# Kernel optimization log

Measured on AMD Instinct MI355X. Metric: run time of the kernel, lower is better.

The kernel has to match this reference:

```python
import jax, jax.numpy as jnp
import numpy as np

N, D, B = 50000, 256, 2048
SIGMA = 1.0
SIGMA2 = SIGMA * SIGMA  # module stores np.square(sigma)


def setup_inputs() -> dict:
    key = jax.random.key(0)
    k1, k2, k3, k4 = jax.random.split(key, 4)
    x = jax.random.normal(k1, (B, D), dtype=jnp.float32)
    data_set = jax.random.normal(k2, (N, D), dtype=jnp.float32)
    # labels are +/-1
    data_labels = jnp.where(jax.random.uniform(k3, (N,)) < 0.5, -1.0, 1.0).astype(jnp.float32)
    # lambdas initialized to ones in the module; use small positive noise around 1/n scale
    lambdas = jax.random.uniform(k4, (N,), dtype=jnp.float32) * (2.0 / N)
    b = jnp.ones((1,), dtype=jnp.float32)
    return {"x": x, "data_set": data_set, "data_labels": data_labels,
            "lambdas": lambdas, "b": b}


def reference(x, data_set, data_labels, lambdas, b):
    x2 = jnp.sum(x * x, axis=1, keepdims=True)            # [B,1]
    s2 = jnp.sum(data_set * data_set, axis=1)             # [N]
    cross = jnp.einsum('bd,nd->bn', x, data_set)          # [B,N]
    sqdist = x2 + s2[None, :] - 2.0 * cross               # [B,N]
    K = jnp.exp(-sqdist / (2.0 * SIGMA2))                 # rbf kernel [B,N]
    w = data_labels * jax.nn.relu(lambdas)                # [N]
    return jnp.tanh(K @ w + b)                            # [B]
```

## Files before the change

### kernel.cpp

```cpp
#include <hip/hip_runtime.h>
#include <hip/hip_bf16.h>
#include <hip/hip_fp8.h>
#include <math.h>

#define NPTS 50000
#define DIM  256
#define BQ   2048
#define NPAD 50048

#define CH   32
#define NCH32 1564
#define NG   64
#define LOG2E 1.4426950408889634f

#define WS_ACC 0
#define WS_X2  2048
#define WS_T   4096
#define WS_SGN 54144
#define WS_XB  104192
#define WS_SB  366336
#define WS_TOTAL_BYTES (6772480ull * 4ull)

#define V1_ACC 0
#define V1_X2  2048
#define V1_S2  4096
#define V1_W   54096

typedef __bf16 bf16x8 __attribute__((ext_vector_type(8)));
typedef __bf16 bf16x4 __attribute__((ext_vector_type(4)));
typedef float  f32x4  __attribute__((ext_vector_type(4)));
typedef float  f32x16 __attribute__((ext_vector_type(16)));
typedef int    i32x4  __attribute__((ext_vector_type(4)));
typedef int    i32x8  __attribute__((ext_vector_type(8)));
typedef unsigned int u32;
typedef unsigned char u8;

__device__ __forceinline__ float fast_exp2(float v) {
#if __has_builtin(__builtin_amdgcn_exp2f)
  return __builtin_amdgcn_exp2f(v);
#else
  return exp2f(v);
#endif
}

__device__ __forceinline__ void async_copy16(const void* g, void* l) {
  __builtin_amdgcn_global_load_lds(
      (const __attribute__((address_space(1))) u32*)g,
      (__attribute__((address_space(3))) u32*)l, 16, 0, 0);
}

__device__ __forceinline__ u32 pack_fp8x4(float4 v) {
#if __has_builtin(__builtin_amdgcn_cvt_pk_fp8_f32)
  int pk = __builtin_amdgcn_cvt_pk_fp8_f32(v.x, v.y, 0, false);
  pk = __builtin_amdgcn_cvt_pk_fp8_f32(v.z, v.w, pk, true);
  return (u32)pk;
#else
  __hip_fp8_e4m3 a(v.x), b(v.y), c(v.z), d(v.w);
  return (u32)a.__x | ((u32)b.__x << 8) | ((u32)c.__x << 16) | ((u32)d.__x << 24);
#endif
}


__global__ __launch_bounds__(256) void svm_precvt10(
    const float* __restrict__ x, const float* __restrict__ s,
    const float* __restrict__ labels, const float* __restrict__ lambdas,
    float* __restrict__ ws) {
  const int wid  = blockIdx.x * 4 + (threadIdx.x >> 6);
  const int lane = threadIdx.x & 63;
  u8* xb8 = (u8*)(ws + WS_XB);
  u8* sb8 = (u8*)(ws + WS_SB);

  if (blockIdx.x < 8) ws[WS_ACC + blockIdx.x * 256 + threadIdx.x] = 0.0f;

  if (wid < NPAD) {
    float4 v = make_float4(0.f, 0.f, 0.f, 0.f);
    if (wid < NPTS)
      v = reinterpret_cast<const float4*>(s + (size_t)wid * DIM)[lane];
    ((u32*)(sb8 + (size_t)wid * DIM))[lane] = pack_fp8x4(v);
    float ss = v.x * v.x + v.y * v.y + v.z * v.z + v.w * v.w;
    #pragma unroll
    for (int off = 32; off > 0; off >>= 1) ss += __shfl_xor(ss, off);
    if (lane == 0) {
      float s2h = 0.5f * LOG2E * ss;
      float lam = (wid < NPTS) ? lambdas[wid] : 0.0f;
      float lab = (wid < NPTS) ? labels[wid] : 1.0f;
      float mag = lam > 0.0f ? lam : 0.0f;
      ws[WS_T + wid]   = (mag > 0.0f) ? s2h - log2f(mag) : __builtin_inff();
      ws[WS_SGN + wid] = lab;
    }
  } else if (wid < NPAD + BQ) {
    int r = wid - NPAD;
    float4 v = reinterpret_cast<const float4*>(x + (size_t)r * DIM)[lane];
    ((u32*)(xb8 + (size_t)r * DIM))[lane] = pack_fp8x4(v);
    float ss = v.x * v.x + v.y * v.y + v.z * v.z + v.w * v.w;
    #pragma unroll
    for (int off = 32; off > 0; off >>= 1) ss += __shfl_xor(ss, off);
    if (lane == 0) ws[WS_X2 + r] = 0.5f * LOG2E * ss;
  }
}

__global__ __launch_bounds__(256, 2) void svm_main20(float* __restrict__ ws) {
  __shared__ u8 sB[3][8192];

  const u8* xb8 = (const u8*)(ws + WS_XB);
  const u8* sb8 = (const u8*)(ws + WS_SB);
  const float* x2g = ws + WS_X2;
  const float* tg  = ws + WS_T;
  const float* sgg = ws + WS_SGN;
  float* accOut    = ws + WS_ACC;

  const int t    = threadIdx.x;
  const int wave = t >> 6;
  const int lane = t & 63;
  const int l32  = lane & 31;
  const int hk   = lane >> 5;
  const int g    = blockIdx.x & (NG - 1);
  const int mt   = blockIdx.x >> 6;
  const int m0   = mt * 256;
  const int c0   = (NCH32 * g) / NG;
  const int c1   = (NCH32 * (g + 1)) / NG;

#define STAGE20(buf, cc)                                                      \
  do {                                                                        \
    _Pragma("unroll")                                                         \
    for (int i = 0; i < 2; ++i) {                                             \
      int p  = wave * 2 + i;                                        \
      int kt = p >> 1;                                              \
      int h  = p & 1;                                                         \
      int r  = h * 16 + (lane >> 2);                                          \
      int q  = (lane & 3) ^ ((r >> 1) & 3);                                   \
      const u8* src = sb8 + (size_t)((cc) * CH + r) * DIM + kt * 64 + q * 16; \
      async_copy16(src, &sB[(buf)][kt * 2048 + h * 1024 + lane * 16]);        \
    }                                                                         \
  } while (0)

  STAGE20(0, c0);
  STAGE20(1, c0 + 1);

  i32x8 afr[2][4];
  #pragma unroll
  for (int mi = 0; mi < 2; ++mi)
    #pragma unroll
    for (int kt = 0; kt < 4; ++kt) {
      const u8* ap = xb8 + (size_t)(m0 + wave * 64 + mi * 32 + l32) * DIM
                         + kt * 64 + hk * 32;
      i32x4 a0 = *reinterpret_cast<const i32x4*>(ap);
      i32x4 a1 = *reinterpret_cast<const i32x4*>(ap + 16);
      afr[mi][kt] = __builtin_shufflevector(a0, a1, 0, 1, 2, 3, 4, 5, 6, 7);
    }
  #pragma unroll
  for (int mi = 0; mi < 2; ++mi)
    #pragma unroll
    for (int kt = 0; kt < 4; ++kt)
      asm volatile("" : "+v"(afr[mi][kt]));

  float runAcc0[16], runAcc1[16];
  #pragma unroll
  for (int i = 0; i < 16; ++i) { runAcc0[i] = 0.0f; runAcc1[i] = 0.0f; }

  asm volatile("s_waitcnt vmcnt(2)" ::: "memory");
  __builtin_amdgcn_s_barrier();

  int cur = 0;
  for (int c = c0; c < c1; ++c) {
    float tt = tg[c * CH + l32];
    float sg = sgg[c * CH + l32];
    __builtin_amdgcn_sched_barrier(0);

    {
      int c2 = c + 2;
      if (c2 < c1) {
        int b2 = cur + 2; if (b2 >= 3) b2 -= 3;
        STAGE20(b2, c2);
      }
    }

    f32x16 acc0 = (f32x16)(0.0f), acc1 = (f32x16)(0.0f);
    const u8* bufB = &sB[cur][0];
    #pragma unroll
    for (int kt = 0; kt < 4; ++kt) {
      int s0 = ((l32 << 2) | (hk << 1)) ^ ((l32 >> 1) & 3);
      const u8* bp = bufB + kt * 2048;
      i32x4 lo = *reinterpret_cast<const i32x4*>(bp + s0 * 16);
      i32x4 hi = *reinterpret_cast<const i32x4*>(bp + (s0 ^ 1) * 16);
      i32x8 bfr = __builtin_shufflevector(lo, hi, 0, 1, 2, 3, 4, 5, 6, 7);
      acc0 = __builtin_amdgcn_mfma_scale_f32_32x32x64_f8f6f4(
          afr[0][kt], bfr, acc0, 0, 0, 0, 0x7F7F7F7F, 0, 0x7F7F7F7F);
      acc1 = __builtin_amdgcn_mfma_scale_f32_32x32x64_f8f6f4(
          afr[1][kt], bfr, acc1, 0, 0, 0, 0x7F7F7F7F, 0, 0x7F7F7F7F);
    }

    #pragma unroll
    for (int reg = 0; reg < 16; ++reg)
      runAcc0[reg] = __builtin_fmaf(
          sg, fast_exp2(__builtin_fmaf(acc0[reg], LOG2E, -tt)), runAcc0[reg]);
    #pragma unroll
    for (int reg = 0; reg < 16; ++reg)
      runAcc1[reg] = __builtin_fmaf(
          sg, fast_exp2(__builtin_fmaf(acc1[reg], LOG2E, -tt)), runAcc1[reg]);

    __builtin_amdgcn_s_barrier();
    asm volatile("" ::: "memory");
    cur = (cur + 1 < 3) ? cur + 1 : 0;
  }

  #pragma unroll
  for (int reg = 0; reg < 16; ++reg) {
    float v = runAcc0[reg];
    v += __shfl_xor(v, 1);
    v += __shfl_xor(v, 2);
    v += __shfl_xor(v, 4);
    v += __shfl_xor(v, 8);
    v += __shfl_xor(v, 16);
    if (l32 == 0) {
      int row = m0 + wave * 64 + (reg & 3) + 8 * (reg >> 2) + 4 * hk;
      atomicAdd(&accOut[row], fast_exp2(-x2g[row]) * v);
    }
  }
  #pragma unroll
  for (int reg = 0; reg < 16; ++reg) {
    float v = runAcc1[reg];
    v += __shfl_xor(v, 1);
    v += __shfl_xor(v, 2);
    v += __shfl_xor(v, 4);
    v += __shfl_xor(v, 8);
    v += __shfl_xor(v, 16);
    if (l32 == 0) {
      int row = m0 + wave * 64 + 32 + (reg & 3) + 8 * (reg >> 2) + 4 * hk;
      atomicAdd(&accOut[row], fast_exp2(-x2g[row]) * v);
    }
  }
#undef STAGE20
}


#define BK 32

__global__ __launch_bounds__(256) void svm_precompute(
    const float* __restrict__ x, const float* __restrict__ s,
    const float* __restrict__ labels, const float* __restrict__ lambdas,
    float* __restrict__ ws) {
  int wid  = blockIdx.x * 4 + (threadIdx.x >> 6);
  int lane = threadIdx.x & 63;
  const float* src;
  if (wid < NPTS)           src = s + (size_t)wid * DIM;
  else if (wid < NPTS + BQ) src = x + (size_t)(wid - NPTS) * DIM;
  else return;
  float4 v = reinterpret_cast<const float4*>(src)[lane];
  float ss = v.x * v.x + v.y * v.y + v.z * v.z + v.w * v.w;
  #pragma unroll
  for (int off = 32; off > 0; off >>= 1) ss += __shfl_xor(ss, off);
  if (lane == 0) {
    if (wid < NPTS) {
      ws[V1_S2 + wid] = ss;
      float lam = lambdas[wid];
      ws[V1_W + wid] = labels[wid] * (lam > 0.0f ? lam : 0.0f);
    } else {
      ws[V1_X2 + (wid - NPTS)] = ss;
    }
  }
}

__global__ __launch_bounds__(256) void svm_main(
    const float* __restrict__ x, const float* __restrict__ s,
    const float* __restrict__ ws) {
  __shared__ __bf16 sA[128 * BK];
  __shared__ __bf16 sB2[128 * BK];

  const int t    = threadIdx.x;
  const int wave = t >> 6;
  const int lane = t & 63;
  const int quad = lane >> 4;
  const int l16  = lane & 15;
  const int wm   = (wave & 1) * 64;
  const int wn   = (wave >> 1) * 64;
  const int bRow0 = blockIdx.y * 128;
  const int n0    = blockIdx.x * 128;

  f32x4 acc[4][4];
  #pragma unroll
  for (int i = 0; i < 4; ++i)
    #pragma unroll
    for (int j = 0; j < 4; ++j)
      acc[i][j] = (f32x4)(0.0f);

  for (int kt = 0; kt < DIM / BK; ++kt) {
    const int k0 = kt * BK;
    __syncthreads();
    #pragma unroll
    for (int i = 0; i < 4; ++i) {
      int slot = t + i * 256;
      int r  = slot >> 3;
      int c4 = slot & 7;
      float4 va = reinterpret_cast<const float4*>(
          x + (size_t)(bRow0 + r) * DIM + k0)[c4];
      bf16x4 ha = { (__bf16)va.x, (__bf16)va.y, (__bf16)va.z, (__bf16)va.w };
      *reinterpret_cast<bf16x4*>(&sA[r * BK + c4 * 4]) = ha;

      int nrow = n0 + r;
      float4 vb = make_float4(0.f, 0.f, 0.f, 0.f);
      if (nrow < NPTS)
        vb = reinterpret_cast<const float4*>(
            s + (size_t)nrow * DIM + k0)[c4];
      bf16x4 hb = { (__bf16)vb.x, (__bf16)vb.y, (__bf16)vb.z, (__bf16)vb.w };
      *reinterpret_cast<bf16x4*>(&sB2[r * BK + c4 * 4]) = hb;
    }
    __syncthreads();

    bf16x8 af[4], bfv[4];
    #pragma unroll
    for (int mi = 0; mi < 4; ++mi)
      af[mi] = *reinterpret_cast<const bf16x8*>(
          &sA[(wm + mi * 16 + l16) * BK + quad * 8]);
    #pragma unroll
    for (int ni = 0; ni < 4; ++ni)
      bfv[ni] = *reinterpret_cast<const bf16x8*>(
          &sB2[(wn + ni * 16 + l16) * BK + quad * 8]);
    #pragma unroll
    for (int mi = 0; mi < 4; ++mi)
      #pragma unroll
      for (int ni = 0; ni < 4; ++ni)
        acc[mi][ni] = __builtin_amdgcn_mfma_f32_16x16x32_bf16(
            af[mi], bfv[ni], acc[mi][ni], 0, 0, 0);
  }

  const float* x2g = ws + V1_X2;
  const float* s2g = ws + V1_S2;
  const float* wg  = ws + V1_W;
  float* accOut    = (float*)ws + V1_ACC;

  float s2v[4], wv[4];
  #pragma unroll
  for (int ni = 0; ni < 4; ++ni) {
    int n = n0 + wn + ni * 16 + l16;
    bool ok = n < NPTS;
    s2v[ni] = ok ? s2g[n] : 0.0f;
    wv[ni]  = ok ? wg[n]  : 0.0f;
  }
  #pragma unroll
  for (int mi = 0; mi < 4; ++mi) {
    const int mbase = wm + mi * 16 + quad * 4;
    #pragma unroll
    for (int reg = 0; reg < 4; ++reg) {
      float x2r = x2g[bRow0 + mbase + reg];
      float ps = 0.0f;
      #pragma unroll
      for (int ni = 0; ni < 4; ++ni) {
        float cc = acc[mi][ni][reg];
        ps += __expf(__builtin_fmaf(-0.5f, x2r + s2v[ni], cc)) * wv[ni];
      }
      ps += __shfl_xor(ps, 1);
      ps += __shfl_xor(ps, 2);
      ps += __shfl_xor(ps, 4);
      ps += __shfl_xor(ps, 8);
      if (l16 == 0) atomicAdd(&accOut[bRow0 + mbase + reg], ps);
    }
  }
}


__global__ __launch_bounds__(256) void svm_finalize(
    const float* __restrict__ ws, const float* __restrict__ bias,
    float* __restrict__ out) {
  int i = blockIdx.x * 256 + threadIdx.x;
  if (i < BQ) out[i] = tanhf(ws[i] + bias[0]);
}

extern "C" void kernel_launch(void* const* d_in, const int* in_sizes, int n_in,
                              void* d_out, int out_size, void* d_ws, size_t ws_size,
                              hipStream_t stream) {
  const float* x       = (const float*)d_in[0];
  const float* s       = (const float*)d_in[1];
  const float* labels  = (const float*)d_in[2];
  const float* lambdas = (const float*)d_in[3];
  const float* bias    = (const float*)d_in[4];
  float* out = (float*)d_out;
  float* ws  = (float*)d_ws;

  if (ws_size >= WS_TOTAL_BYTES) {
    svm_precvt10<<<(NPAD + BQ + 3) / 4, 256, 0, stream>>>(x, s, labels, lambdas, ws);
    svm_main20<<<8 * NG, 256, 0, stream>>>(ws);
  } else {
    hipMemsetAsync(ws, 0, BQ * sizeof(float), stream);
    svm_precompute<<<(NPTS + BQ + 3) / 4, 256, 0, stream>>>(x, s, labels, lambdas, ws);
    dim3 grid(391, BQ / 128);
    svm_main<<<grid, 256, 0, stream>>>(x, s, ws);
  }
  svm_finalize<<<BQ / 256, 256, 0, stream>>>(ws, bias, out);
}
```

Measured before the change: 144.9 us.

## Process two chunks per barrier with a four-buffer LDS ring

The main loop now handles two 32-point chunks per iteration and uses a 4-deep LDS ring instead of 3, so it needs half as many workgroup barriers and has more independent MFMA/exp work between syncs. A tail handles an odd chunk count. The precompute step also switches log2f to the hardware log intrinsic, which is slightly less accurate. LDS use per block grows from 24KB to 32KB, which may matter for occupancy at two blocks per CU.

```diff
diff --git a/kernel.cpp b/kernel.cpp
--- a/kernel.cpp
+++ b/kernel.cpp
@@ -40,6 +40,14 @@
   return __builtin_amdgcn_exp2f(v);
 #else
   return exp2f(v);
+#endif
+}
+
+__device__ __forceinline__ float fast_log2(float v) {
+#if __has_builtin(__builtin_amdgcn_logf)
+  return __builtin_amdgcn_logf(v);
+#else
+  return __log2f(v);
 #endif
 }
 
@@ -85,7 +93,7 @@
       float lam = (wid < NPTS) ? lambdas[wid] : 0.0f;
       float lab = (wid < NPTS) ? labels[wid] : 1.0f;
       float mag = lam > 0.0f ? lam : 0.0f;
-      ws[WS_T + wid]   = (mag > 0.0f) ? s2h - log2f(mag) : __builtin_inff();
+      ws[WS_T + wid]   = (mag > 0.0f) ? s2h - fast_log2(mag) : __builtin_inff();
       ws[WS_SGN + wid] = lab;
     }
   } else if (wid < NPAD + BQ) {
@@ -99,8 +107,8 @@
   }
 }
 
-__global__ __launch_bounds__(256, 2) void svm_main20(float* __restrict__ ws) {
-  __shared__ u8 sB[3][8192];
+__global__ __launch_bounds__(256, 2) void svm_main23(float* __restrict__ ws) {
+  __shared__ u8 sB[4][8192];
 
   const u8* xb8 = (const u8*)(ws + WS_XB);
   const u8* sb8 = (const u8*)(ws + WS_SB);
@@ -120,7 +128,7 @@
   const int c0   = (NCH32 * g) / NG;
   const int c1   = (NCH32 * (g + 1)) / NG;
 
-#define STAGE20(buf, cc)                                                      \
+#define STAGE23(buf, cc)                                                      \
   do {                                                                        \
     _Pragma("unroll")                                                         \
     for (int i = 0; i < 2; ++i) {                                             \
@@ -134,8 +142,36 @@
     }                                                                         \
   } while (0)
 
-  STAGE20(0, c0);
-  STAGE20(1, c0 + 1);
+#define CHUNK23(BUFIDX, CC)                                                   \
+  do {                                                                        \
+    f32x16 acc0 = (f32x16)(0.0f), acc1 = (f32x16)(0.0f);                      \
+    const u8* bufB = &sB[(BUFIDX)][0];                                        \
+    _Pragma("unroll")                                                         \
+    for (int kt = 0; kt < 4; ++kt) {                                          \
+      int s0 = ((l32 << 2) | (hk << 1)) ^ ((l32 >> 1) & 3);                   \
+      const u8* bp = bufB + kt * 2048;                                        \
+      i32x4 lo = *reinterpret_cast<const i32x4*>(bp + s0 * 16);               \
+      i32x4 hi = *reinterpret_cast<const i32x4*>(bp + (s0 ^ 1) * 16);         \
+      i32x8 bfr = __builtin_shufflevector(lo, hi, 0, 1, 2, 3, 4, 5, 6, 7);    \
+      acc0 = __builtin_amdgcn_mfma_scale_f32_32x32x64_f8f6f4(                 \
+          afr[0][kt], bfr, acc0, 0, 0, 0, 0x7F7F7F7F, 0, 0x7F7F7F7F);         \
+      acc1 = __builtin_amdgcn_mfma_scale_f32_32x32x64_f8f6f4(                 \
+          afr[1][kt], bfr, acc1, 0, 0, 0, 0x7F7F7F7F, 0, 0x7F7F7F7F);         \
+    }                                                                         \
+    _Pragma("unroll")                                                         \
+    for (int reg = 0; reg < 16; ++reg)                                        \
+      runAcc0[reg] = __builtin_fmaf(                                          \
+          sg_##CC, fast_exp2(__builtin_fmaf(acc0[reg], LOG2E, -tt_##CC)),     \
+          runAcc0[reg]);                                                      \
+    _Pragma("unroll")                                                         \
+    for (int reg = 0; reg < 16; ++reg)                                        \
+      runAcc1[reg] = __builtin_fmaf(                                          \
+          sg_##CC, fast_exp2(__builtin_fmaf(acc1[reg], LOG2E, -tt_##CC)),     \
+          runAcc1[reg]);                                                      \
+  } while (0)
+
+  STAGE23(0, c0);
+  STAGE23(1, c0 + 1);
 
   i32x8 afr[2][4];
   #pragma unroll
@@ -162,46 +198,29 @@
   __builtin_amdgcn_s_barrier();
 
   int cur = 0;
-  for (int c = c0; c < c1; ++c) {
-    float tt = tg[c * CH + l32];
-    float sg = sgg[c * CH + l32];
+  int c = c0;
+  for (; c + 1 < c1; c += 2) {
+    float tt_a = tg[c * CH + l32];
+    float sg_a = sgg[c * CH + l32];
     __builtin_amdgcn_sched_barrier(0);
-
-    {
-      int c2 = c + 2;
-      if (c2 < c1) {
-        int b2 = cur + 2; if (b2 >= 3) b2 -= 3;
-        STAGE20(b2, c2);
-      }
-    }
-
-    f32x16 acc0 = (f32x16)(0.0f), acc1 = (f32x16)(0.0f);
-    const u8* bufB = &sB[cur][0];
-    #pragma unroll
-    for (int kt = 0; kt < 4; ++kt) {
-      int s0 = ((l32 << 2) | (hk << 1)) ^ ((l32 >> 1) & 3);
-      const u8* bp = bufB + kt * 2048;
-      i32x4 lo = *reinterpret_cast<const i32x4*>(bp + s0 * 16);
-      i32x4 hi = *reinterpret_cast<const i32x4*>(bp + (s0 ^ 1) * 16);
-      i32x8 bfr = __builtin_shufflevector(lo, hi, 0, 1, 2, 3, 4, 5, 6, 7);
-      acc0 = __builtin_amdgcn_mfma_scale_f32_32x32x64_f8f6f4(
-          afr[0][kt], bfr, acc0, 0, 0, 0, 0x7F7F7F7F, 0, 0x7F7F7F7F);
-      acc1 = __builtin_amdgcn_mfma_scale_f32_32x32x64_f8f6f4(
-          afr[1][kt], bfr, acc1, 0, 0, 0, 0x7F7F7F7F, 0, 0x7F7F7F7F);
-    }
-
-    #pragma unroll
-    for (int reg = 0; reg < 16; ++reg)
-      runAcc0[reg] = __builtin_fmaf(
-          sg, fast_exp2(__builtin_fmaf(acc0[reg], LOG2E, -tt)), runAcc0[reg]);
-    #pragma unroll
-    for (int reg = 0; reg < 16; ++reg)
-      runAcc1[reg] = __builtin_fmaf(
-          sg, fast_exp2(__builtin_fmaf(acc1[reg], LOG2E, -tt)), runAcc1[reg]);
+    if (c + 2 < c1) { int b = (cur + 2) & 3; STAGE23(b, c + 2); }
+
+    float tt_b = tg[(c + 1) * CH + l32];
+    float sg_b = sgg[(c + 1) * CH + l32];
+    __builtin_amdgcn_sched_barrier(0);
+    if (c + 3 < c1) { int b = (cur + 3) & 3; STAGE23(b, c + 3); }
+
+    CHUNK23(cur, a);
+    CHUNK23((cur + 1) & 3, b);
 
     __builtin_amdgcn_s_barrier();
     asm volatile("" ::: "memory");
-    cur = (cur + 1 < 3) ? cur + 1 : 0;
+    cur = (cur + 2) & 3;
+  }
+  if (c < c1) {
+    float tt_a = tg[c * CH + l32];
+    float sg_a = sgg[c * CH + l32];
+    CHUNK23(cur, a);
   }
 
   #pragma unroll
@@ -230,7 +249,8 @@
       atomicAdd(&accOut[row], fast_exp2(-x2g[row]) * v);
     }
   }
-#undef STAGE20
+#undef CHUNK23
+#undef STAGE23
 }
 
 
@@ -379,12 +399,13 @@
 
   if (ws_size >= WS_TOTAL_BYTES) {
     svm_precvt10<<<(NPAD + BQ + 3) / 4, 256, 0, stream>>>(x, s, labels, lambdas, ws);
-    svm_main20<<<8 * NG, 256, 0, stream>>>(ws);
+    svm_main23<<<8 * NG, 256, 0, stream>>>(ws);
+    svm_finalize<<<BQ / 256, 256, 0, stream>>>(ws, bias, out);
   } else {
     hipMemsetAsync(ws, 0, BQ * sizeof(float), stream);
     svm_precompute<<<(NPTS + BQ + 3) / 4, 256, 0, stream>>>(x, s, labels, lambdas, ws);
     dim3 grid(391, BQ / 128);
     svm_main<<<grid, 256, 0, stream>>>(x, s, ws);
-  }
-  svm_finalize<<<BQ / 256, 256, 0, stream>>>(ws, bias, out);
-}
+    svm_finalize<<<BQ / 256, 256, 0, stream>>>(ws, bias, out);
+  }
+}
```

Result: no change. 144.9 us (+0.0%).
